# Kernel optimization log

Hardware: AMD Instinct MI355X
Metric: run time of the kernel (lower is better)

## Reference

```python
import jax, jax.numpy as jnp
import numpy as np

B, N, C = 2, 2048, 1024
H = 16
D = C // H  # head_dim = 64
SCALE = D ** -0.5


def setup_inputs() -> dict:
    key = jax.random.key(0)
    k1, k2, k3, k4 = jax.random.split(key, 4)
    x = jax.random.normal(k1, (B, N, C), dtype=jnp.float32)
    # nn.Linear(in_dim, 3*out_dim, bias=False): store as [in, 3*out] for x @ W
    w_qkv = jax.random.normal(k2, (C, 3 * C), dtype=jnp.float32) * (C ** -0.5)
    w_proj = jax.random.normal(k3, (C, C), dtype=jnp.float32) * (C ** -0.5)
    b_proj = jax.random.normal(k4, (C,), dtype=jnp.float32) * 0.01
    return {"x": x, "w_qkv": w_qkv, "w_proj": w_proj, "b_proj": b_proj}


def reference(x, w_qkv, w_proj, b_proj):
    b, n, c = x.shape
    # QKV projection -> [3, B, H, N, D]
    qkv = (x @ w_qkv).reshape(b, n, 3, H, D).transpose(2, 0, 3, 1, 4)
    q, k, v = qkv[0], qkv[1], qkv[2]
    # scaled dot-product attention, full [B, H, N, N] scores as in original
    attn = jax.nn.softmax(jnp.einsum('bhqd,bhkd->bhqk', q * SCALE, k), axis=-1)
    out = jnp.einsum('bhqk,bhkd->bhqd', attn, v)  # [B, H, N, D]
    out = out.transpose(0, 2, 1, 3).reshape(b, n, c)
    return out @ w_proj + b_proj
```

## Files before the change

### kernel.cpp

```cpp
#include <hip/hip_runtime.h>

typedef unsigned short u16;
typedef float f32x4 __attribute__((ext_vector_type(4)));
typedef short bf16x8 __attribute__((ext_vector_type(8)));
typedef u16 u16x4 __attribute__((ext_vector_type(4)));
typedef u16 u16x8 __attribute__((ext_vector_type(8)));
typedef __bf16 bfr4 __attribute__((ext_vector_type(4)));

#define BB 2
#define NN 2048
#define CC 1024
#define HH 16
#define DD 64
#define MM (BB * NN)
#define NQKV (3 * CC)
#define QSCALE 0.18033688011112042f

#if __has_builtin(__builtin_amdgcn_exp2f)
#define EXP2(x) __builtin_amdgcn_exp2f(x)
#else
#define EXP2(x) exp2f(x)
#endif

__device__ __forceinline__ u16 f2bf(float f) {
    unsigned u = __float_as_uint(f);
    u += 0x7FFFu + ((u >> 16) & 1u);
    return (u16)(u >> 16);
}

__device__ __forceinline__ void ld_lds16(const u16* g, u16* l) {
    __builtin_amdgcn_global_load_lds(
        (const __attribute__((address_space(1))) unsigned int*)g,
        (__attribute__((address_space(3))) unsigned int*)l, 16, 0, 0);
}

__global__ __launch_bounds__(256) void k_tobf(const float* __restrict__ in,
                                              u16* __restrict__ out, int n) {
    int i = (blockIdx.x * 256 + threadIdx.x) * 8;
    if (i >= n) return;
    float4 a = *(const float4*)(in + i);
    float4 b = *(const float4*)(in + i + 4);
    u16x8 o;
    o[0] = f2bf(a.x); o[1] = f2bf(a.y); o[2] = f2bf(a.z); o[3] = f2bf(a.w);
    o[4] = f2bf(b.x); o[5] = f2bf(b.y); o[6] = f2bf(b.z); o[7] = f2bf(b.w);
    *(u16x8*)(out + i) = o;
}

__global__ __launch_bounds__(256) void k_tcast(const float* __restrict__ in,
                                               u16* __restrict__ out,
                                               int K, int Nn) {
    __shared__ float tile[32][33];
    int t = threadIdx.x, tx = t & 31, ty = t >> 5;
    int n0 = blockIdx.x * 32, k0 = blockIdx.y * 32;
#pragma unroll
    for (int r = 0; r < 32; r += 8)
        tile[ty + r][tx] = in[(size_t)(k0 + ty + r) * Nn + n0 + tx];
    __syncthreads();
#pragma unroll
    for (int r = 0; r < 32; r += 8)
        out[(size_t)(n0 + ty + r) * K + k0 + tx] = f2bf(tile[tx][ty + r]);
}

template <int MODE>
__global__ __launch_bounds__(256) void k_gemm(
    const u16* __restrict__ A, const u16* __restrict__ B,
    u16* __restrict__ Qb, u16* __restrict__ Kb, u16* __restrict__ Vb,
    const float* __restrict__ bias, float* __restrict__ Cout) {
    const int Kd = 1024;
    __shared__ __align__(16) u16 Ah[128][32];
    __shared__ __align__(16) u16 Bh[128][32];

    int t = threadIdx.x;
    int wave = t >> 6, lane = t & 63;
    int quad = lane >> 4, l16 = lane & 15;
    int wm = (wave >> 1) * 64, wn = (wave & 1) * 64;
    int m0 = blockIdx.y * 128, n0 = blockIdx.x * 128;

    int strow0 = wave * 16 + (lane >> 2);
    int stdst  = (lane & 3) * 8;
    int stsrc  = ((lane & 3) ^ ((lane >> 3) & 3)) * 8;
    int cfrag = (quad ^ ((l16 >> 1) & 3)) * 8;

    f32x4 acc[4][4];
#pragma unroll
    for (int i = 0; i < 4; i++)
#pragma unroll
        for (int j = 0; j < 4; j++) acc[i][j] = f32x4{0.f, 0.f, 0.f, 0.f};

    for (int k0 = 0; k0 < Kd; k0 += 32) {
        __syncthreads();
#pragma unroll
        for (int ii = 0; ii < 2; ii++) {
            int row = strow0 + ii * 64;
            ld_lds16(A + (size_t)(m0 + row) * Kd + k0 + stsrc, &Ah[row][stdst]);
            ld_lds16(B + (size_t)(n0 + row) * Kd + k0 + stsrc, &Bh[row][stdst]);
        }
        __syncthreads();

        bf16x8 af[4], bf[4];
#pragma unroll
        for (int i = 0; i < 4; i++) {
            af[i] = *(const bf16x8*)&Ah[wm + i * 16 + l16][cfrag];
            bf[i] = *(const bf16x8*)&Bh[wn + i * 16 + l16][cfrag];
        }
#pragma unroll
        for (int mi = 0; mi < 4; mi++)
#pragma unroll
            for (int ni = 0; ni < 4; ni++)
                acc[mi][ni] = __builtin_amdgcn_mfma_f32_16x16x32_bf16(
                    af[mi], bf[ni], acc[mi][ni], 0, 0, 0);
    }

#pragma unroll
    for (int mi = 0; mi < 4; mi++)
#pragma unroll
        for (int ni = 0; ni < 4; ni++)
#pragma unroll
            for (int r = 0; r < 4; r++) {
                int grow = m0 + wm + mi * 16 + quad * 4 + r;
                int gcol = n0 + wn + ni * 16 + l16;
                float v = acc[mi][ni][r];
                if (MODE == 0) {
                    int three = gcol >> 10, rem = gcol & 1023;
                    int h = rem >> 6, d = rem & 63;
                    int bb = grow >> 11, nn = grow & 2047;
                    if (three == 0) {
                        Qb[((size_t)(bb * HH + h) * NN + nn) * DD + d] = f2bf(v * QSCALE);
                    } else if (three == 1) {
                        Kb[((size_t)(bb * HH + h) * NN + nn) * DD + d] = f2bf(v);
                    } else {
                        Vb[((size_t)(bb * HH + h) * DD + d) * NN + nn] = f2bf(v);
                    }
                } else {
                    Cout[(size_t)grow * CC + gcol] = v + bias[gcol];
                }
            }
}

__global__ __launch_bounds__(128) void k_attn(const u16* __restrict__ Qb,
                                              const u16* __restrict__ Kb,
                                              const u16* __restrict__ VbT,
                                              u16* __restrict__ Ob) {
    __shared__ __align__(16) u16 Ks[64][64];
    __shared__ __align__(16) u16 Vs[64][64];
    __shared__ __align__(16) u16 Ps[2][64][64];

    int t = threadIdx.x, wave = t >> 6, lane = t & 63;
    int quad = lane >> 4, l16 = lane & 15;
    int bh = blockIdx.y, q0 = blockIdx.x * 128;
    const size_t kbase = (size_t)bh * NN * DD;
    const size_t vbase = (size_t)bh * DD * NN;

    bf16x8 qf[4][2];
#pragma unroll
    for (int qj = 0; qj < 4; qj++) {
        int qrow = q0 + wave * 64 + qj * 16 + l16;
        qf[qj][0] = *(const bf16x8*)&Qb[kbase + (size_t)qrow * DD + quad * 8];
        qf[qj][1] = *(const bf16x8*)&Qb[kbase + (size_t)qrow * DD + 32 + quad * 8];
    }

    bf16x8 ones;
#pragma unroll
    for (int j = 0; j < 8; j++) ones[j] = (short)0x3F80;

    f32x4 o[4][4];
    f32x4 accl[4];
#pragma unroll
    for (int i = 0; i < 4; i++) {
        accl[i] = f32x4{0.f, 0.f, 0.f, 0.f};
#pragma unroll
        for (int j = 0; j < 4; j++) o[i][j] = f32x4{0.f, 0.f, 0.f, 0.f};
    }

    int stgrp  = lane & 7;
    int stsrc  = (stgrp ^ (lane >> 3)) * 8;
    int strow0 = wave * 8 + (lane >> 3);
    int cf0 = (quad ^ (l16 & 7)) * 8;
    int cf1 = ((4 + quad) ^ (l16 & 7)) * 8;
    int psw = (quad & 1) * 4;

    for (int c = 0; c < NN / 64; c++) {
        __syncthreads();
#pragma unroll
        for (int ii = 0; ii < 4; ii++) {
            int row = strow0 + ii * 16;
            ld_lds16(&Kb[kbase + (size_t)(c * 64 + row) * DD + stsrc], &Ks[row][stgrp * 8]);
            ld_lds16(&VbT[vbase + (size_t)row * NN + c * 64 + stsrc], &Vs[row][stgrp * 8]);
        }
        __syncthreads();

        bf16x8 kf[4][2];
#pragma unroll
        for (int kt = 0; kt < 4; kt++) {
            kf[kt][0] = *(const bf16x8*)&Ks[kt * 16 + l16][cf0];
            kf[kt][1] = *(const bf16x8*)&Ks[kt * 16 + l16][cf1];
        }

#pragma unroll
        for (int qj = 0; qj < 4; qj++) {
            f32x4 s[4];
#pragma unroll
            for (int kt = 0; kt < 4; kt++) {
                f32x4 z = f32x4{0.f, 0.f, 0.f, 0.f};
                z = __builtin_amdgcn_mfma_f32_16x16x32_bf16(kf[kt][0], qf[qj][0], z, 0, 0, 0);
                z = __builtin_amdgcn_mfma_f32_16x16x32_bf16(kf[kt][1], qf[qj][1], z, 0, 0, 0);
                s[kt] = z;
            }
#pragma unroll
            for (int kt = 0; kt < 4; kt++) {
                bfr4 pk;
#pragma unroll
                for (int r = 0; r < 4; r++) pk[r] = (__bf16)EXP2(s[kt][r]);
                int og = 2 * kt + (quad >> 1);
                *(bfr4*)&Ps[wave][qj * 16 + l16][(og ^ (l16 & 7)) * 8 + psw] = pk;
            }
        }
        __asm__ volatile("s_waitcnt lgkmcnt(0)" ::: "memory");

        bf16x8 pb[4][2];
#pragma unroll
        for (int qj = 0; qj < 4; qj++) {
            pb[qj][0] = *(const bf16x8*)&Ps[wave][qj * 16 + l16][cf0];
            pb[qj][1] = *(const bf16x8*)&Ps[wave][qj * 16 + l16][cf1];
            accl[qj] = __builtin_amdgcn_mfma_f32_16x16x32_bf16(ones, pb[qj][0], accl[qj], 0, 0, 0);
            accl[qj] = __builtin_amdgcn_mfma_f32_16x16x32_bf16(ones, pb[qj][1], accl[qj], 0, 0, 0);
        }
#pragma unroll
        for (int dt = 0; dt < 4; dt++) {
            bf16x8 vf0 = *(const bf16x8*)&Vs[dt * 16 + l16][cf0];
            bf16x8 vf1 = *(const bf16x8*)&Vs[dt * 16 + l16][cf1];
#pragma unroll
            for (int qj = 0; qj < 4; qj++) {
                o[dt][qj] = __builtin_amdgcn_mfma_f32_16x16x32_bf16(vf0, pb[qj][0], o[dt][qj], 0, 0, 0);
                o[dt][qj] = __builtin_amdgcn_mfma_f32_16x16x32_bf16(vf1, pb[qj][1], o[dt][qj], 0, 0, 0);
            }
        }
    }

    int b = bh >> 4, h = bh & 15;
#pragma unroll
    for (int qj = 0; qj < 4; qj++) {
        float inv = 1.f / accl[qj][0];
        int grow = b * NN + q0 + wave * 64 + qj * 16 + l16;
#pragma unroll
        for (int dt = 0; dt < 4; dt++) {
            u16x4 hv;
#pragma unroll
            for (int r = 0; r < 4; r++) hv[r] = f2bf(o[dt][qj][r] * inv);
            int gcol = h * DD + dt * 16 + quad * 4;
            *(u16x4*)&Ob[(size_t)grow * CC + gcol] = hv;
        }
    }
}

extern "C" void kernel_launch(void* const* d_in, const int* in_sizes, int n_in,
                              void* d_out, int out_size, void* d_ws, size_t ws_size,
                              hipStream_t stream) {
    const float* x      = (const float*)d_in[0];
    const float* w_qkv  = (const float*)d_in[1];
    const float* w_proj = (const float*)d_in[2];
    const float* b_proj = (const float*)d_in[3];
    float* out = (float*)d_out;

    u16* p = (u16*)d_ws;
    u16* Xb = p; p += (size_t)MM * CC;
    u16* Wq = p; p += (size_t)NQKV * CC;
    u16* Wp = p; p += (size_t)CC * CC;
    u16* Qb = p; p += (size_t)MM * CC;
    u16* Kb = p; p += (size_t)MM * CC;
    u16* Vb = p; p += (size_t)MM * CC;
    u16* Ob = p; p += (size_t)MM * CC;

    k_tobf<<<(MM * CC) / (256 * 8), 256, 0, stream>>>(x, Xb, MM * CC);
    k_tcast<<<dim3(NQKV / 32, CC / 32), 256, 0, stream>>>(w_qkv, Wq, CC, NQKV);
    k_tcast<<<dim3(CC / 32, CC / 32), 256, 0, stream>>>(w_proj, Wp, CC, CC);
    k_gemm<0><<<dim3(NQKV / 128, MM / 128), 256, 0, stream>>>(
        Xb, Wq, Qb, Kb, Vb, nullptr, nullptr);
    k_attn<<<dim3(NN / 128, BB * HH), 128, 0, stream>>>(Qb, Kb, Vb, Ob);
    k_gemm<1><<<dim3(CC / 128, MM / 128), 256, 0, stream>>>(
        Ob, Wp, nullptr, nullptr, nullptr, b_proj, out);
}
```

Before: 214.2 us.

## Split attention KV range across two blocks and add reduction kernel

```diff
diff --git a/kernel.cpp b/kernel.cpp
--- a/kernel.cpp
+++ b/kernel.cpp
@@ -26,6 +26,9 @@
     unsigned u = __float_as_uint(f);
     u += 0x7FFFu + ((u >> 16) & 1u);
     return (u16)(u >> 16);
+}
+__device__ __forceinline__ float bf2f(u16 b) {
+    return __uint_as_float(((unsigned)b) << 16);
 }
 
 __device__ __forceinline__ void ld_lds16(const u16* g, u16* l) {
@@ -137,24 +140,26 @@
             }
 }
 
-__global__ __launch_bounds__(128) void k_attn(const u16* __restrict__ Qb,
+__global__ __launch_bounds__(256) void k_attn(const u16* __restrict__ Qb,
                                               const u16* __restrict__ Kb,
                                               const u16* __restrict__ VbT,
-                                              u16* __restrict__ Ob) {
+                                              u16* __restrict__ Opart,
+                                              float* __restrict__ Lpart) {
     __shared__ __align__(16) u16 Ks[64][64];
     __shared__ __align__(16) u16 Vs[64][64];
-    __shared__ __align__(16) u16 Ps[2][64][64];
+    __shared__ __align__(16) u16 Ps[4][64][64];
 
     int t = threadIdx.x, wave = t >> 6, lane = t & 63;
     int quad = lane >> 4, l16 = lane & 15;
-    int bh = blockIdx.y, q0 = blockIdx.x * 128;
+    int bh = blockIdx.y, sp = blockIdx.z;
+    int q0 = blockIdx.x * 256 + wave * 64;
     const size_t kbase = (size_t)bh * NN * DD;
     const size_t vbase = (size_t)bh * DD * NN;
 
     bf16x8 qf[4][2];
 #pragma unroll
     for (int qj = 0; qj < 4; qj++) {
-        int qrow = q0 + wave * 64 + qj * 16 + l16;
+        int qrow = q0 + qj * 16 + l16;
         qf[qj][0] = *(const bf16x8*)&Qb[kbase + (size_t)qrow * DD + quad * 8];
         qf[qj][1] = *(const bf16x8*)&Qb[kbase + (size_t)qrow * DD + 32 + quad * 8];
     }
@@ -174,16 +179,16 @@
 
     int stgrp  = lane & 7;
     int stsrc  = (stgrp ^ (lane >> 3)) * 8;
-    int strow0 = wave * 8 + (lane >> 3);
+    int strow0 = wave * 16 + (lane >> 3);
     int cf0 = (quad ^ (l16 & 7)) * 8;
     int cf1 = ((4 + quad) ^ (l16 & 7)) * 8;
     int psw = (quad & 1) * 4;
 
-    for (int c = 0; c < NN / 64; c++) {
+    for (int c = sp * 16; c < sp * 16 + 16; c++) {
         __syncthreads();
 #pragma unroll
-        for (int ii = 0; ii < 4; ii++) {
-            int row = strow0 + ii * 16;
+        for (int ii = 0; ii < 2; ii++) {
+            int row = strow0 + ii * 8;
             ld_lds16(&Kb[kbase + (size_t)(c * 64 + row) * DD + stsrc], &Ks[row][stgrp * 8]);
             ld_lds16(&VbT[vbase + (size_t)row * NN + c * 64 + stsrc], &Vs[row][stgrp * 8]);
         }
@@ -240,17 +245,35 @@
     int b = bh >> 4, h = bh & 15;
 #pragma unroll
     for (int qj = 0; qj < 4; qj++) {
-        float inv = 1.f / accl[qj][0];
-        int grow = b * NN + q0 + wave * 64 + qj * 16 + l16;
+        int grow = b * NN + q0 + qj * 16 + l16;
+        size_t orow = ((size_t)sp * MM + grow) * CC;
 #pragma unroll
         for (int dt = 0; dt < 4; dt++) {
             u16x4 hv;
 #pragma unroll
-            for (int r = 0; r < 4; r++) hv[r] = f2bf(o[dt][qj][r] * inv);
-            int gcol = h * DD + dt * 16 + quad * 4;
-            *(u16x4*)&Ob[(size_t)grow * CC + gcol] = hv;
-        }
-    }
+            for (int r = 0; r < 4; r++) hv[r] = f2bf(o[dt][qj][r]);
+            *(u16x4*)&Opart[orow + h * DD + dt * 16 + quad * 4] = hv;
+        }
+        if (quad == 0)
+            Lpart[((size_t)sp * MM + grow) * HH + h] = accl[qj][0];
+    }
+}
+
+__global__ __launch_bounds__(256) void k_reduce(const u16* __restrict__ Op,
+                                                const float* __restrict__ Lp,
+                                                u16* __restrict__ Ob) {
+    size_t i = ((size_t)blockIdx.x * 256 + threadIdx.x) * 8;
+    int m = (int)(i >> 10);
+    int c = (int)(i & 1023);
+    int h = c >> 6;
+    float l = Lp[(size_t)m * HH + h] + Lp[(size_t)(MM + m) * HH + h];
+    float inv = 1.f / l;
+    u16x8 p0 = *(const u16x8*)&Op[i];
+    u16x8 p1 = *(const u16x8*)&Op[(size_t)MM * CC + i];
+    u16x8 o;
+#pragma unroll
+    for (int j = 0; j < 8; j++) o[j] = f2bf((bf2f(p0[j]) + bf2f(p1[j])) * inv);
+    *(u16x8*)&Ob[i] = o;
 }
 
 extern "C" void kernel_launch(void* const* d_in, const int* in_sizes, int n_in,
@@ -270,13 +293,16 @@
     u16* Kb = p; p += (size_t)MM * CC;
     u16* Vb = p; p += (size_t)MM * CC;
     u16* Ob = p; p += (size_t)MM * CC;
+    u16* Opart = p; p += (size_t)2 * MM * CC;
+    float* Lpart = (float*)p;
 
     k_tobf<<<(MM * CC) / (256 * 8), 256, 0, stream>>>(x, Xb, MM * CC);
     k_tcast<<<dim3(NQKV / 32, CC / 32), 256, 0, stream>>>(w_qkv, Wq, CC, NQKV);
     k_tcast<<<dim3(CC / 32, CC / 32), 256, 0, stream>>>(w_proj, Wp, CC, CC);
     k_gemm<0><<<dim3(NQKV / 128, MM / 128), 256, 0, stream>>>(
         Xb, Wq, Qb, Kb, Vb, nullptr, nullptr);
-    k_attn<<<dim3(NN / 128, BB * HH), 128, 0, stream>>>(Qb, Kb, Vb, Ob);
+    k_attn<<<dim3(NN / 256, BB * HH, 2), 256, 0, stream>>>(Qb, Kb, Vb, Opart, Lpart);
+    k_reduce<<<(MM * CC) / (256 * 8), 256, 0, stream>>>(Opart, Lpart, Ob);
     k_gemm<1><<<dim3(CC / 128, MM / 128), 256, 0, stream>>>(
         Ob, Wp, nullptr, nullptr, nullptr, b_proj, out);
 }
```

Measured after the change: 223.3 us. 4.3% more time.
